# Performance work log

Measured on AMD Instinct MI355X. Metric: run time of the kernel, lower is better.

## Reference

```python
import jax, jax.numpy as jnp
import numpy as np


def _conv(x, w, b=None, pad=0):
    # x: [B,C,H,W], w: [O,I,kh,kw]
    y = jax.lax.conv_general_dilated(
        x, w, window_strides=(1, 1), padding=[(pad, pad), (pad, pad)],
        dimension_numbers=('NCHW', 'OIHW', 'NCHW'))
    if b is not None:
        y = y + b[None, :, None, None]
    return y


def _resb(x, w1, w2):
    h = _conv(x, w1, pad=1)
    h = jax.nn.leaky_relu(h, 0.1)
    h = _conv(h, w2, pad=1)
    return h + x


def setup_inputs() -> dict:
    key = jax.random.key(0)
    ks = jax.random.split(key, 16)
    B, C, H, W, K = 2, 64, 128, 256, 16
    s = 0.05
    return {
        'x_left': jax.random.normal(ks[0], (B, C, H, W), jnp.float32),
        'x_right': jax.random.normal(ks[1], (B, C, H, W), jnp.float32),
        'xxs': jax.random.randint(ks[2], (B, H * W, K), 0, H, jnp.int32),
        'yys': jax.random.randint(ks[3], (B, H * W, K), 0, W, jnp.int32),
        'is_training': 0,
        'rb_w1': jax.random.normal(ks[4], (C, C, 3, 3), jnp.float32) * s,
        'rb_w2': jax.random.normal(ks[5], (C, C, 3, 3), jnp.float32) * s,
        'b1_w': jax.random.normal(ks[6], (C, C, 1, 1), jnp.float32) * s,
        'b1_b': jax.random.normal(ks[7], (C,), jnp.float32) * s,
        'b2_w': jax.random.normal(ks[8], (C, C, 1, 1), jnp.float32) * s,
        'b2_b': jax.random.normal(ks[9], (C,), jnp.float32) * s,
        'b3_w': jax.random.normal(ks[10], (C, C, 1, 1), jnp.float32) * s,
        'b3_b': jax.random.normal(ks[11], (C,), jnp.float32) * s,
        'fus_w': jax.random.normal(ks[12], (C, 2 * C, 1, 1), jnp.float32) * s,
        'fus_b': jax.random.normal(ks[13], (C,), jnp.float32) * s,
    }


def reference(x_left, x_right, xxs, yys, is_training,
              rb_w1, rb_w2, b1_w, b1_b, b2_w, b2_b, b3_w, b3_b, fus_w, fus_b):
    B, C, H, W = x_left.shape
    HW = H * W
    K = xxs.shape[-1]

    buf_l = _resb(x_left, rb_w1, rb_w2)
    buf_r = _resb(x_right, rb_w1, rb_w2)

    Q = _conv(buf_l, b1_w, b1_b)   # [B,C,H,W]
    S = _conv(buf_r, b2_w, b2_b)
    R = _conv(buf_r, b3_w, b3_b)

    # per-pixel gather: S[b,:,Pos_x,Pos_y] -> flat index into H*W
    flat = (xxs.astype(jnp.int32) * W + yys.astype(jnp.int32)).reshape(B, HW * K)  # [B,HW*K]
    Sf = S.reshape(B, C, HW)
    Rf = R.reshape(B, C, HW)
    Key = jnp.take_along_axis(Sf, flat[:, None, :], axis=2).reshape(B, C, HW, K)
    Val = jnp.take_along_axis(Rf, flat[:, None, :], axis=2).reshape(B, C, HW, K)

    Qv = Q.transpose(0, 2, 3, 1).reshape(B, HW, C)           # [B,HW,C]
    score = jnp.einsum('bpc,bcpk->bpk', Qv, Key)             # [B,HW,K]
    M = jax.nn.softmax(score, axis=-1)                       # [B,HW,K]
    buf = jnp.einsum('bpk,bckp->bpc', M, Val.transpose(0, 1, 3, 2))  # [B,HW,C]
    buf = buf.reshape(B, H, W, C).transpose(0, 3, 1, 2)      # [B,C,H,W]

    out = _conv(jnp.concatenate([buf, x_left], axis=1), fus_w, fus_b)
    M_right_to_left = M[:, :, None, :]                       # [B,HW,1,K] as in torch
    if is_training == 1:
        return out
    return (out, M_right_to_left)
```

## Files before the change

### kernel.cpp

```cpp
#include <hip/hip_runtime.h>

#define HH 128
#define WW 256
#define CH 64
#define HWP (HH * WW)

typedef __attribute__((ext_vector_type(8))) __bf16 bf16x8;
typedef __attribute__((ext_vector_type(16))) float float16;

__device__ __forceinline__ unsigned short f2bf(float f) {
    unsigned u = __float_as_uint(f);
    u += 0x7fffu + ((u >> 16) & 1u);
    return (unsigned short)(u >> 16);
}
__device__ __forceinline__ float bf2f(unsigned short u) {
    return __uint_as_float((unsigned)u << 16);
}

__global__ __launch_bounds__(256) void prep_toT_k(
    const float* __restrict__ xl, const float* __restrict__ xr,
    const float* __restrict__ w1, const float* __restrict__ w2,
    const float* __restrict__ b1w, const float* __restrict__ b2w,
    const float* __restrict__ b3w, const float* __restrict__ fusw,
    unsigned short* __restrict__ XT, unsigned short* __restrict__ wB)
{
    const int tid = threadIdx.x;
    if (blockIdx.x < 2048) {
        __shared__ __align__(16) unsigned short sT[64 * 68];
        const int side = blockIdx.x >> 10;
        const int i0   = blockIdx.x & 1023;
        const int gp0  = i0 * 64;
        const int b    = gp0 >> 15;
        const int pofs = gp0 & (HWP - 1);
        const float* in = (side ? xr : xl) + (size_t)b * CH * HWP + pofs;

        for (int i = tid; i < 4096; i += 256) {
            int ci = i >> 6, px = i & 63;
            sT[px * 68 + ci] = f2bf(in[(size_t)ci * HWP + px]);
        }
        __syncthreads();
        const int px = tid >> 2, q = tid & 3;
        unsigned short* op = XT + ((size_t)(side * 2 + b) * HWP + pofs + px) * 64;
#pragma unroll
        for (int r = 0; r < 2; ++r)
            *(uint4*)&op[(q * 2 + r) * 8] = *(uint4*)&sT[px * 68 + (q * 2 + r) * 8];
        return;
    }

    int e = (blockIdx.x - 2048) * 256 + tid;
    float val;
    if (e < 73728) {
        const float* w = (e < 36864) ? w1 : w2;
        int t = (e < 36864) ? e : e - 36864;
        int j = t & 7, L = (t >> 3) & 63, nb = (t >> 9) & 1, kc = t >> 10;
        int k  = kc * 16 + (L >> 5) * 8 + j;
        int n  = nb * 32 + (L & 31);
        int kd = k >> 6, ci = k & 63;
        val = w[(n * 64 + ci) * 9 + kd];
    } else {
        int t = e - 73728;
        if (t < 4096) {
            int j = t & 7, L = (t >> 3) & 63, i3 = t >> 9;
            int nt = i3 & 1, kc = i3 >> 1;
            int n = nt * 32 + (L & 31), k = kc * 16 + (L >> 5) * 8 + j;
            val = b1w[n * 64 + k];
        } else if (t < 12288) {
            t -= 4096;
            int j = t & 7, L = (t >> 3) & 63, i3 = t >> 9;
            int nt = i3 & 3, kc = i3 >> 2;
            int n = nt * 32 + (L & 31), k = kc * 16 + (L >> 5) * 8 + j;
            val = (n < 64) ? b2w[n * 64 + k] : b3w[(n - 64) * 64 + k];
        } else {
            t -= 12288;
            int j = t & 7, L = (t >> 3) & 63, i3 = t >> 9;
            int nt = i3 & 1, kc = i3 >> 1;
            int n = nt * 32 + (L & 31), k = kc * 16 + (L >> 5) * 8 + j;
            val = fusw[n * 128 + k];
        }
    }
    wB[e] = f2bf(val);
}

__device__ __forceinline__ void stage_halo(
    unsigned short* sA, const unsigned short* inT, int x0, int y, int tid)
{
    for (int i = tid; i < 1584; i += 256) {
        int cell = i >> 3, j = i & 7;
        int row = cell / 66, col = cell - row * 66;
        int gy = y + row - 1, gx = x0 + col - 1;
        uint4 v = make_uint4(0, 0, 0, 0);
        if ((unsigned)gy < HH && (unsigned)gx < WW)
            v = *(const uint4*)&inT[(size_t)(gy * WW + gx) * 64 + j * 8];
        *(uint4*)&sA[(row * 66 + col) * 68 + j * 8] = v;
    }
}

__global__ __launch_bounds__(256) void conv1_k(
    const unsigned short* __restrict__ XT, const unsigned short* __restrict__ wB,
    unsigned short* __restrict__ H1T)
{
    __shared__ __align__(16) unsigned short sA[4 * 66 * 68];

    const int tid = threadIdx.x;
    const int x0  = blockIdx.x * 64;
    const int y0  = blockIdx.y * 2;
    const int sb  = blockIdx.z;
    const unsigned short* inT = XT + (size_t)sb * HWP * 64;

    for (int i = tid; i < 2112; i += 256) {
        int cell = i >> 3, j = i & 7;
        int row = cell / 66, col = cell - row * 66;
        int gy = y0 + row - 1, gx = x0 + col - 1;
        uint4 v = make_uint4(0, 0, 0, 0);
        if ((unsigned)gy < HH && (unsigned)gx < WW)
            v = *(const uint4*)&inT[(size_t)(gy * WW + gx) * 64 + j * 8];
        *(uint4*)&sA[(row * 66 + col) * 68 + j * 8] = v;
    }
    __syncthreads();

    const int lane = tid & 63, wv = tid >> 6;
    const int h = wv & 1, nw = wv >> 1;
    const int m = lane & 31, kg = lane >> 5;
    const int pxl = h * 32 + m;

    float16 acc0, acc1;
#pragma unroll
    for (int i = 0; i < 16; ++i) { acc0[i] = 0.f; acc1[i] = 0.f; }

#pragma unroll
    for (int kc = 0; kc < 36; ++kc) {
        const int kd = kc >> 2, hh = kc & 3;
        const int dy = kd / 3, dx = kd - dy * 3;
        bf16x8 bfg = *(const bf16x8*)&wB[((kc * 2 + nw) * 64 + lane) * 8];
        const int base = (dy * 66 + pxl + dx) * 68 + hh * 16 + kg * 8;
        bf16x8 af0 = *(const bf16x8*)&sA[base];
        bf16x8 af1 = *(const bf16x8*)&sA[base + 66 * 68];
        acc0 = __builtin_amdgcn_mfma_f32_32x32x16_bf16(af0, bfg, acc0, 0, 0, 0);
        acc1 = __builtin_amdgcn_mfma_f32_32x32x16_bf16(af1, bfg, acc1, 0, 0, 0);
    }

    __syncthreads();
    unsigned short* sCb = sA;
    const int n = nw * 32 + (lane & 31);
#pragma unroll
    for (int r = 0; r < 16; ++r) {
        int prl = h * 32 + (r & 3) + 8 * (r >> 2) + 4 * kg;
        float v0 = acc0[r]; v0 = v0 > 0.f ? v0 : 0.1f * v0;
        float v1 = acc1[r]; v1 = v1 > 0.f ? v1 : 0.1f * v1;
        sCb[prl * 68 + n] = f2bf(v0);
        sCb[(64 + prl) * 68 + n] = f2bf(v1);
    }
    __syncthreads();

    const int px2 = tid >> 1, q = tid & 1;
    const int rr = px2 >> 6, px = px2 & 63;
    unsigned short* op = H1T + ((size_t)sb * HWP + (y0 + rr) * WW + x0 + px) * 64 + q * 32;
#pragma unroll
    for (int j = 0; j < 4; ++j)
        *(uint4*)&op[j * 8] = *(uint4*)&sCb[px2 * 68 + q * 32 + j * 8];
}

__global__ __launch_bounds__(256) void conv2_k(
    const unsigned short* __restrict__ H1T, const unsigned short* __restrict__ XT,
    const unsigned short* __restrict__ wB2, const unsigned short* __restrict__ wQ,
    const unsigned short* __restrict__ wSR, const float* __restrict__ b1b,
    const float* __restrict__ b2b, const float* __restrict__ b3b,
    unsigned short* __restrict__ QT, unsigned short* __restrict__ ST,
    unsigned short* __restrict__ RT)
{
    __shared__ __align__(16) unsigned short sA[3 * 66 * 68];

    const int tid = threadIdx.x;
    const int x0  = blockIdx.x * 64;
    const int y   = blockIdx.y;
    const int sb  = blockIdx.z;
    const int side = sb >> 1, b = sb & 1;
    const unsigned short* inT = H1T + (size_t)sb * HWP * 64;

    stage_halo(sA, inT, x0, y, tid);
    __syncthreads();

    const int lane = tid & 63, wv = tid >> 6;
    const int mw = wv & 1, nw = wv >> 1;
    const int m = lane & 31, kg = lane >> 5;
    const int px_l = mw * 32 + m;

    float16 acc;
#pragma unroll
    for (int i = 0; i < 16; ++i) acc[i] = 0.f;

#pragma unroll
    for (int kc = 0; kc < 36; ++kc) {
        const int kd = kc >> 2, h = kc & 3;
        const int dy = kd / 3, dx = kd - dy * 3;
        bf16x8 af = *(const bf16x8*)&sA[((dy * 66 + px_l + dx) * 68) + h * 16 + kg * 8];
        bf16x8 bf = *(const bf16x8*)&wB2[((kc * 2 + nw) * 64 + lane) * 8];
        acc = __builtin_amdgcn_mfma_f32_32x32x16_bf16(af, bf, acc, 0, 0, 0);
    }

    __syncthreads();
    unsigned short* sCb = sA;
    unsigned short* sC2 = sA + 4352;
    const int n = nw * 32 + (lane & 31);
    const unsigned short* xres = XT + (size_t)sb * HWP * 64;
#pragma unroll
    for (int r = 0; r < 16; ++r) {
        int pr = mw * 32 + (r & 3) + 8 * (r >> 2) + 4 * kg;
        float xv = bf2f(xres[(size_t)(y * WW + x0 + pr) * 64 + n]);
        sCb[pr * 68 + n] = f2bf(acc[r] + xv);
    }
    __syncthreads();

    if (side == 0) {
        float16 a2;
#pragma unroll
        for (int i = 0; i < 16; ++i) a2[i] = 0.f;
#pragma unroll
        for (int kc = 0; kc < 4; ++kc) {
            bf16x8 af = *(const bf16x8*)&sCb[px_l * 68 + kc * 16 + kg * 8];
            bf16x8 bf = *(const bf16x8*)&wQ[((kc * 2 + nw) * 64 + lane) * 8];
            a2 = __builtin_amdgcn_mfma_f32_32x32x16_bf16(af, bf, a2, 0, 0, 0);
        }
        float bv = b1b[n];
#pragma unroll
        for (int r = 0; r < 16; ++r) {
            int pr = mw * 32 + (r & 3) + 8 * (r >> 2) + 4 * kg;
            sC2[pr * 68 + n] = f2bf(a2[r] + bv);
        }
        __syncthreads();
        const int px = tid >> 2, q = tid & 3;
        unsigned short* op = QT + ((size_t)b * HWP + y * WW + x0 + px) * 64;
#pragma unroll
        for (int r = 0; r < 2; ++r)
            *(uint4*)&op[(q * 2 + r) * 8] = *(uint4*)&sC2[px * 68 + (q * 2 + r) * 8];
    } else {
        float16 a2[2];
#pragma unroll
        for (int t = 0; t < 2; ++t)
#pragma unroll
            for (int i = 0; i < 16; ++i) a2[t][i] = 0.f;
#pragma unroll
        for (int kc = 0; kc < 4; ++kc) {
            bf16x8 af = *(const bf16x8*)&sCb[px_l * 68 + kc * 16 + kg * 8];
#pragma unroll
            for (int t = 0; t < 2; ++t) {
                int nt = nw * 2 + t;
                bf16x8 bf = *(const bf16x8*)&wSR[((kc * 4 + nt) * 64 + lane) * 8];
                a2[t] = __builtin_amdgcn_mfma_f32_32x32x16_bf16(af, bf, a2[t], 0, 0, 0);
            }
        }
#pragma unroll
        for (int t = 0; t < 2; ++t) {
            int nn = (nw * 2 + t) * 32 + (lane & 31);
            float bv = (nn < 64) ? b2b[nn] : b3b[nn - 64];
#pragma unroll
            for (int r = 0; r < 16; ++r) {
                int pr = mw * 32 + (r & 3) + 8 * (r >> 2) + 4 * kg;
                sC2[pr * 132 + nn] = f2bf(a2[t][r] + bv);
            }
        }
        __syncthreads();
        const int px = tid >> 2, q = tid & 3;
        const size_t prow = (size_t)b * HWP + y * WW + x0 + px;
        unsigned short* op = ((q < 2) ? ST : RT) + prow * 64 + (q & 1) * 32;
#pragma unroll
        for (int j = 0; j < 4; ++j)
            *(uint4*)&op[j * 8] = *(uint4*)&sC2[px * 132 + q * 32 + j * 8];
    }
}

__global__ __launch_bounds__(512) void attn_fuse_k(
    const unsigned short* __restrict__ QT, const unsigned short* __restrict__ ST,
    const unsigned short* __restrict__ RT, const int* __restrict__ xxs,
    const int* __restrict__ yys, const unsigned short* __restrict__ XT,
    const unsigned short* __restrict__ wfrag, const float* __restrict__ bias,
    float* __restrict__ out, float* __restrict__ Mout)
{
    __shared__ __align__(16) unsigned char smem[64 * 68 * 4];
    unsigned short* sBuf = (unsigned short*)smem;
    unsigned short* sXT  = (unsigned short*)smem + 64 * 68;
    float*          sC   = (float*)smem;

    const int tid  = threadIdx.x;
    const int lane = tid & 63;
    const int wv   = tid >> 6;

    const int blk = blockIdx.x;
    const int b   = (blk & 4) ? 1 : 0;
    const int sub = (blk >> 3) * 4 + (blk & 3);
    const int pofs = sub * 64;
    const size_t gp0   = (size_t)b * HWP + pofs;
    const size_t bbase = (size_t)b * HWP;

    {
        const unsigned short* xlT = XT + gp0 * 64;
        int px = tid >> 3, j = tid & 7;
        *(uint4*)&sXT[px * 68 + j * 8] = *(const uint4*)&xlT[(size_t)px * 64 + j * 8];
    }

    const int k = lane & 15, cq = lane >> 4;
    for (int it = 0; it < 8; ++it) {
        const int pl = wv * 8 + it;
        const size_t gp = gp0 + pl;

        const int flat = xxs[gp * 16 + k] * WW + yys[gp * 16 + k];

        const unsigned short* srow = ST + (bbase + (size_t)flat) * 64 + cq * 16;
        const unsigned short* qrow = QT + gp * 64 + cq * 16;
        float s = 0.f;
#pragma unroll
        for (int hh = 0; hh < 2; ++hh) {
            uint4 sv = *(const uint4*)(srow + hh * 8);
            uint4 qv = *(const uint4*)(qrow + hh * 8);
            const unsigned* sa = (const unsigned*)&sv;
            const unsigned* qa = (const unsigned*)&qv;
#pragma unroll
            for (int d = 0; d < 4; ++d) {
                s = fmaf(__uint_as_float(sa[d] << 16),
                         __uint_as_float(qa[d] << 16), s);
                s = fmaf(__uint_as_float(sa[d] & 0xffff0000u),
                         __uint_as_float(qa[d] & 0xffff0000u), s);
            }
        }
        s += __shfl_xor(s, 16, 64);
        s += __shfl_xor(s, 32, 64);

        float mx = s;
#pragma unroll
        for (int mm = 1; mm <= 8; mm <<= 1) mx = fmaxf(mx, __shfl_xor(mx, mm, 64));
        const float e = __expf(s - mx);
        float sum = e;
#pragma unroll
        for (int mm = 1; mm <= 8; mm <<= 1) sum += __shfl_xor(sum, mm, 64);
        const float mval = e * (1.f / sum);

        if (lane < 16) Mout[gp * 16 + lane] = mval;

        const unsigned short* rbase = RT + bbase * 64;
        float acc = 0.f;
#pragma unroll
        for (int kk = 0; kk < 16; ++kk) {
            int   fi = __builtin_amdgcn_readlane(flat, kk);
            float mk = __uint_as_float(
                __builtin_amdgcn_readlane(__float_as_uint(mval), kk));
            acc = fmaf(mk, bf2f(rbase[(size_t)fi * 64 + lane]), acc);
        }
        sBuf[pl * 68 + lane] = f2bf(acc);
    }
    __syncthreads();

    float16 facc;
#pragma unroll
    for (int i = 0; i < 16; ++i) facc[i] = 0.f;
    const int mw = wv & 1, nw = (wv >> 1) & 1;
    const int m = lane & 31, kg = lane >> 5;
    const int px_l = mw * 32 + m;

    if (tid < 256) {
#pragma unroll
        for (int kc = 0; kc < 8; ++kc) {
            const unsigned short* asrc = (kc < 4)
                ? &sBuf[px_l * 68 + kc * 16 + kg * 8]
                : &sXT[px_l * 68 + (kc - 4) * 16 + kg * 8];
            bf16x8 af = *(const bf16x8*)asrc;
            bf16x8 bf = *(const bf16x8*)&wfrag[((kc * 2 + nw) * 64 + lane) * 8];
            facc = __builtin_amdgcn_mfma_f32_32x32x16_bf16(af, bf, facc, 0, 0, 0);
        }
    }
    __syncthreads();

    if (tid < 256) {
        const int co_l = nw * 32 + (lane & 31);
#pragma unroll
        for (int r = 0; r < 16; ++r) {
            int pr = mw * 32 + (r & 3) + 8 * (r >> 2) + 4 * kg;
            sC[co_l * 68 + pr] = facc[r];
        }
    }
    __syncthreads();

    if (tid < 256) {
        const int co = tid >> 2, p0 = (tid & 3) * 16;
        const float bv = bias[co];
        float* op = out + ((size_t)b * CH + co) * HWP + pofs + p0;
#pragma unroll
        for (int q = 0; q < 4; ++q) {
            float4 v = *(float4*)&sC[co * 68 + p0 + q * 4];
            v.x += bv; v.y += bv; v.z += bv; v.w += bv;
            *(float4*)&op[q * 4] = v;
        }
    }
}

extern "C" void kernel_launch(void* const* d_in, const int* in_sizes, int n_in,
                              void* d_out, int out_size, void* d_ws, size_t ws_size,
                              hipStream_t stream)
{
    const float* x_left  = (const float*)d_in[0];
    const float* x_right = (const float*)d_in[1];
    const int*   xxs     = (const int*)d_in[2];
    const int*   yys     = (const int*)d_in[3];
    const float* rb_w1   = (const float*)d_in[5];
    const float* rb_w2   = (const float*)d_in[6];
    const float* b1_w    = (const float*)d_in[7];
    const float* b1_b    = (const float*)d_in[8];
    const float* b2_w    = (const float*)d_in[9];
    const float* b2_b    = (const float*)d_in[10];
    const float* b3_w    = (const float*)d_in[11];
    const float* b3_b    = (const float*)d_in[12];
    const float* fus_w   = (const float*)d_in[13];
    const float* fus_b   = (const float*)d_in[14];

    float* out  = (float*)d_out;
    float* Mout = out + (size_t)2 * CH * HWP;

    unsigned short* ws2 = (unsigned short*)d_ws;
    unsigned short* XT   = ws2;
    unsigned short* H1T  = ws2 + 8388608;
    unsigned short* QT   = ws2 + 16777216;
    unsigned short* ST   = ws2 + 20971520;
    unsigned short* RT   = ws2 + 25165824;
    unsigned short* wB   = ws2 + 29360128;

    prep_toT_k<<<2416, 256, 0, stream>>>(x_left, x_right, rb_w1, rb_w2,
                                         b1_w, b2_w, b3_w, fus_w, XT, wB);

    conv1_k<<<dim3(4, 64, 4), 256, 0, stream>>>(XT, wB, H1T);
    conv2_k<<<dim3(4, 128, 4), 256, 0, stream>>>(H1T, XT, wB + 36864, wB + 73728,
                                                 wB + 77824, b1_b, b2_b, b3_b,
                                                 QT, ST, RT);

    attn_fuse_k<<<1024, 512, 0, stream>>>(QT, ST, RT, xxs, yys, XT,
                                          wB + 86016, fus_b, out, Mout);
}
```

Baseline: 197.2 us.

## Use 512-thread blocks with per-wave row split in both 3x3 conv kernels

```diff
diff --git a/kernel.cpp b/kernel.cpp
--- a/kernel.cpp
+++ b/kernel.cpp
@@ -81,33 +81,10 @@
     wB[e] = f2bf(val);
 }
 
-__device__ __forceinline__ void stage_halo(
-    unsigned short* sA, const unsigned short* inT, int x0, int y, int tid)
-{
-    for (int i = tid; i < 1584; i += 256) {
-        int cell = i >> 3, j = i & 7;
-        int row = cell / 66, col = cell - row * 66;
-        int gy = y + row - 1, gx = x0 + col - 1;
-        uint4 v = make_uint4(0, 0, 0, 0);
-        if ((unsigned)gy < HH && (unsigned)gx < WW)
-            v = *(const uint4*)&inT[(size_t)(gy * WW + gx) * 64 + j * 8];
-        *(uint4*)&sA[(row * 66 + col) * 68 + j * 8] = v;
-    }
-}
-
-__global__ __launch_bounds__(256) void conv1_k(
-    const unsigned short* __restrict__ XT, const unsigned short* __restrict__ wB,
-    unsigned short* __restrict__ H1T)
-{
-    __shared__ __align__(16) unsigned short sA[4 * 66 * 68];
-
-    const int tid = threadIdx.x;
-    const int x0  = blockIdx.x * 64;
-    const int y0  = blockIdx.y * 2;
-    const int sb  = blockIdx.z;
-    const unsigned short* inT = XT + (size_t)sb * HWP * 64;
-
-    for (int i = tid; i < 2112; i += 256) {
+__device__ __forceinline__ void stage_halo4(
+    unsigned short* sA, const unsigned short* inT, int x0, int y0, int tid)
+{
+    for (int i = tid; i < 2112; i += 512) {
         int cell = i >> 3, j = i & 7;
         int row = cell / 66, col = cell - row * 66;
         int gy = y0 + row - 1, gx = x0 + col - 1;
@@ -116,27 +93,39 @@
             v = *(const uint4*)&inT[(size_t)(gy * WW + gx) * 64 + j * 8];
         *(uint4*)&sA[(row * 66 + col) * 68 + j * 8] = v;
     }
+}
+
+__global__ __launch_bounds__(512) void conv1_k(
+    const unsigned short* __restrict__ XT, const unsigned short* __restrict__ wB,
+    unsigned short* __restrict__ H1T)
+{
+    __shared__ __align__(16) unsigned short sA[4 * 66 * 68];
+
+    const int tid = threadIdx.x;
+    const int x0  = blockIdx.x * 64;
+    const int y0  = blockIdx.y * 2;
+    const int sb  = blockIdx.z;
+    const unsigned short* inT = XT + (size_t)sb * HWP * 64;
+
+    stage_halo4(sA, inT, x0, y0, tid);
     __syncthreads();
 
     const int lane = tid & 63, wv = tid >> 6;
-    const int h = wv & 1, nw = wv >> 1;
+    const int rr = wv & 1, mw = (wv >> 1) & 1, nw = wv >> 2;
     const int m = lane & 31, kg = lane >> 5;
-    const int pxl = h * 32 + m;
-
-    float16 acc0, acc1;
-#pragma unroll
-    for (int i = 0; i < 16; ++i) { acc0[i] = 0.f; acc1[i] = 0.f; }
+    const int pxl = mw * 32 + m;
+
+    float16 acc;
+#pragma unroll
+    for (int i = 0; i < 16; ++i) acc[i] = 0.f;
 
 #pragma unroll
     for (int kc = 0; kc < 36; ++kc) {
         const int kd = kc >> 2, hh = kc & 3;
         const int dy = kd / 3, dx = kd - dy * 3;
-        bf16x8 bfg = *(const bf16x8*)&wB[((kc * 2 + nw) * 64 + lane) * 8];
-        const int base = (dy * 66 + pxl + dx) * 68 + hh * 16 + kg * 8;
-        bf16x8 af0 = *(const bf16x8*)&sA[base];
-        bf16x8 af1 = *(const bf16x8*)&sA[base + 66 * 68];
-        acc0 = __builtin_amdgcn_mfma_f32_32x32x16_bf16(af0, bfg, acc0, 0, 0, 0);
-        acc1 = __builtin_amdgcn_mfma_f32_32x32x16_bf16(af1, bfg, acc1, 0, 0, 0);
+        bf16x8 af = *(const bf16x8*)&sA[((rr + dy) * 66 + pxl + dx) * 68 + hh * 16 + kg * 8];
+        bf16x8 bf = *(const bf16x8*)&wB[((kc * 2 + nw) * 64 + lane) * 8];
+        acc = __builtin_amdgcn_mfma_f32_32x32x16_bf16(af, bf, acc, 0, 0, 0);
     }
 
     __syncthreads();
@@ -144,23 +133,21 @@
     const int n = nw * 32 + (lane & 31);
 #pragma unroll
     for (int r = 0; r < 16; ++r) {
-        int prl = h * 32 + (r & 3) + 8 * (r >> 2) + 4 * kg;
-        float v0 = acc0[r]; v0 = v0 > 0.f ? v0 : 0.1f * v0;
-        float v1 = acc1[r]; v1 = v1 > 0.f ? v1 : 0.1f * v1;
-        sCb[prl * 68 + n] = f2bf(v0);
-        sCb[(64 + prl) * 68 + n] = f2bf(v1);
-    }
-    __syncthreads();
-
-    const int px2 = tid >> 1, q = tid & 1;
-    const int rr = px2 >> 6, px = px2 & 63;
-    unsigned short* op = H1T + ((size_t)sb * HWP + (y0 + rr) * WW + x0 + px) * 64 + q * 32;
-#pragma unroll
-    for (int j = 0; j < 4; ++j)
-        *(uint4*)&op[j * 8] = *(uint4*)&sCb[px2 * 68 + q * 32 + j * 8];
-}
-
-__global__ __launch_bounds__(256) void conv2_k(
+        int pr = rr * 64 + mw * 32 + (r & 3) + 8 * (r >> 2) + 4 * kg;
+        float v = acc[r];
+        v = v > 0.f ? v : 0.1f * v;
+        sCb[pr * 68 + n] = f2bf(v);
+    }
+    __syncthreads();
+
+    const int px2 = tid >> 2, q = tid & 3;
+    const int orow = px2 >> 6, px = px2 & 63;
+    unsigned short* op = H1T + ((size_t)sb * HWP + (y0 + orow) * WW + x0 + px) * 64 + q * 16;
+    *(uint4*)&op[0] = *(uint4*)&sCb[px2 * 68 + q * 16];
+    *(uint4*)&op[8] = *(uint4*)&sCb[px2 * 68 + q * 16 + 8];
+}
+
+__global__ __launch_bounds__(512) void conv2_k(
     const unsigned short* __restrict__ H1T, const unsigned short* __restrict__ XT,
     const unsigned short* __restrict__ wB2, const unsigned short* __restrict__ wQ,
     const unsigned short* __restrict__ wSR, const float* __restrict__ b1b,
@@ -168,22 +155,22 @@
     unsigned short* __restrict__ QT, unsigned short* __restrict__ ST,
     unsigned short* __restrict__ RT)
 {
-    __shared__ __align__(16) unsigned short sA[3 * 66 * 68];
+    __shared__ __align__(16) unsigned short sA[4 * 66 * 68];
 
     const int tid = threadIdx.x;
     const int x0  = blockIdx.x * 64;
-    const int y   = blockIdx.y;
+    const int y0  = blockIdx.y * 2;
     const int sb  = blockIdx.z;
     const int side = sb >> 1, b = sb & 1;
     const unsigned short* inT = H1T + (size_t)sb * HWP * 64;
 
-    stage_halo(sA, inT, x0, y, tid);
+    stage_halo4(sA, inT, x0, y0, tid);
     __syncthreads();
 
     const int lane = tid & 63, wv = tid >> 6;
-    const int mw = wv & 1, nw = wv >> 1;
+    const int rr = wv & 1, mw = (wv >> 1) & 1, nw = wv >> 2;
     const int m = lane & 31, kg = lane >> 5;
-    const int px_l = mw * 32 + m;
+    const int pxl = mw * 32 + m;
 
     float16 acc;
 #pragma unroll
@@ -191,25 +178,29 @@
 
 #pragma unroll
     for (int kc = 0; kc < 36; ++kc) {
-        const int kd = kc >> 2, h = kc & 3;
+        const int kd = kc >> 2, hh = kc & 3;
         const int dy = kd / 3, dx = kd - dy * 3;
-        bf16x8 af = *(const bf16x8*)&sA[((dy * 66 + px_l + dx) * 68) + h * 16 + kg * 8];
+        bf16x8 af = *(const bf16x8*)&sA[((rr + dy) * 66 + pxl + dx) * 68 + hh * 16 + kg * 8];
         bf16x8 bf = *(const bf16x8*)&wB2[((kc * 2 + nw) * 64 + lane) * 8];
         acc = __builtin_amdgcn_mfma_f32_32x32x16_bf16(af, bf, acc, 0, 0, 0);
     }
 
     __syncthreads();
     unsigned short* sCb = sA;
-    unsigned short* sC2 = sA + 4352;
+    unsigned short* sC2 = sA + 8704;
     const int n = nw * 32 + (lane & 31);
     const unsigned short* xres = XT + (size_t)sb * HWP * 64;
 #pragma unroll
     for (int r = 0; r < 16; ++r) {
-        int pr = mw * 32 + (r & 3) + 8 * (r >> 2) + 4 * kg;
-        float xv = bf2f(xres[(size_t)(y * WW + x0 + pr) * 64 + n]);
+        int pr = rr * 64 + mw * 32 + (r & 3) + 8 * (r >> 2) + 4 * kg;
+        float xv = bf2f(xres[(size_t)((y0 + (pr >> 6)) * WW + x0 + (pr & 63)) * 64 + n]);
         sCb[pr * 68 + n] = f2bf(acc[r] + xv);
     }
     __syncthreads();
+
+    const int px2 = tid >> 2, q = tid & 3;
+    const int orow = px2 >> 6, px = px2 & 63;
+    const size_t prow = (size_t)b * HWP + (y0 + orow) * WW + x0 + px;
 
     if (side == 0) {
         float16 a2;
@@ -217,55 +208,68 @@
         for (int i = 0; i < 16; ++i) a2[i] = 0.f;
 #pragma unroll
         for (int kc = 0; kc < 4; ++kc) {
-            bf16x8 af = *(const bf16x8*)&sCb[px_l * 68 + kc * 16 + kg * 8];
+            bf16x8 af = *(const bf16x8*)&sCb[(rr * 64 + pxl) * 68 + kc * 16 + kg * 8];
             bf16x8 bf = *(const bf16x8*)&wQ[((kc * 2 + nw) * 64 + lane) * 8];
             a2 = __builtin_amdgcn_mfma_f32_32x32x16_bf16(af, bf, a2, 0, 0, 0);
         }
         float bv = b1b[n];
 #pragma unroll
         for (int r = 0; r < 16; ++r) {
-            int pr = mw * 32 + (r & 3) + 8 * (r >> 2) + 4 * kg;
+            int pr = rr * 64 + mw * 32 + (r & 3) + 8 * (r >> 2) + 4 * kg;
             sC2[pr * 68 + n] = f2bf(a2[r] + bv);
         }
         __syncthreads();
-        const int px = tid >> 2, q = tid & 3;
-        unsigned short* op = QT + ((size_t)b * HWP + y * WW + x0 + px) * 64;
-#pragma unroll
-        for (int r = 0; r < 2; ++r)
-            *(uint4*)&op[(q * 2 + r) * 8] = *(uint4*)&sC2[px * 68 + (q * 2 + r) * 8];
+        unsigned short* op = QT + prow * 64 + q * 16;
+        *(uint4*)&op[0] = *(uint4*)&sC2[px2 * 68 + q * 16];
+        *(uint4*)&op[8] = *(uint4*)&sC2[px2 * 68 + q * 16 + 8];
     } else {
-        float16 a2[2];
-#pragma unroll
-        for (int t = 0; t < 2; ++t)
-#pragma unroll
-            for (int i = 0; i < 16; ++i) a2[t][i] = 0.f;
+        float16 a2;
+#pragma unroll
+        for (int i = 0; i < 16; ++i) a2[i] = 0.f;
 #pragma unroll
         for (int kc = 0; kc < 4; ++kc) {
-            bf16x8 af = *(const bf16x8*)&sCb[px_l * 68 + kc * 16 + kg * 8];
-#pragma unroll
-            for (int t = 0; t < 2; ++t) {
-                int nt = nw * 2 + t;
-                bf16x8 bf = *(const bf16x8*)&wSR[((kc * 4 + nt) * 64 + lane) * 8];
-                a2[t] = __builtin_amdgcn_mfma_f32_32x32x16_bf16(af, bf, a2[t], 0, 0, 0);
+            bf16x8 af = *(const bf16x8*)&sCb[(rr * 64 + pxl) * 68 + kc * 16 + kg * 8];
+            bf16x8 bf = *(const bf16x8*)&wSR[((kc * 4 + nw) * 64 + lane) * 8];
+            a2 = __builtin_amdgcn_mfma_f32_32x32x16_bf16(af, bf, a2, 0, 0, 0);
+        }
+        {
+            float bv = b2b[n];
+#pragma unroll
+            for (int r = 0; r < 16; ++r) {
+                int pr = rr * 64 + mw * 32 + (r & 3) + 8 * (r >> 2) + 4 * kg;
+                sC2[pr * 68 + n] = f2bf(a2[r] + bv);
             }
         }
-#pragma unroll
-        for (int t = 0; t < 2; ++t) {
-            int nn = (nw * 2 + t) * 32 + (lane & 31);
-            float bv = (nn < 64) ? b2b[nn] : b3b[nn - 64];
+        __syncthreads();
+        {
+            unsigned short* op = ST + prow * 64 + q * 16;
+            *(uint4*)&op[0] = *(uint4*)&sC2[px2 * 68 + q * 16];
+            *(uint4*)&op[8] = *(uint4*)&sC2[px2 * 68 + q * 16 + 8];
+        }
+        __syncthreads();
+
+#pragma unroll
+        for (int i = 0; i < 16; ++i) a2[i] = 0.f;
+#pragma unroll
+        for (int kc = 0; kc < 4; ++kc) {
+            bf16x8 af = *(const bf16x8*)&sCb[(rr * 64 + pxl) * 68 + kc * 16 + kg * 8];
+            bf16x8 bf = *(const bf16x8*)&wSR[((kc * 4 + 2 + nw) * 64 + lane) * 8];
+            a2 = __builtin_amdgcn_mfma_f32_32x32x16_bf16(af, bf, a2, 0, 0, 0);
+        }
+        {
+            float bv = b3b[n];
 #pragma unroll
             for (int r = 0; r < 16; ++r) {
-                int pr = mw * 32 + (r & 3) + 8 * (r >> 2) + 4 * kg;
-                sC2[pr * 132 + nn] = f2bf(a2[t][r] + bv);
+                int pr = rr * 64 + mw * 32 + (r & 3) + 8 * (r >> 2) + 4 * kg;
+                sC2[pr * 68 + n] = f2bf(a2[r] + bv);
             }
         }
         __syncthreads();
-        const int px = tid >> 2, q = tid & 3;
-        const size_t prow = (size_t)b * HWP + y * WW + x0 + px;
-        unsigned short* op = ((q < 2) ? ST : RT) + prow * 64 + (q & 1) * 32;
-#pragma unroll
-        for (int j = 0; j < 4; ++j)
-            *(uint4*)&op[j * 8] = *(uint4*)&sC2[px * 132 + q * 32 + j * 8];
+        {
+            unsigned short* op = RT + prow * 64 + q * 16;
+            *(uint4*)&op[0] = *(uint4*)&sC2[px2 * 68 + q * 16];
+            *(uint4*)&op[8] = *(uint4*)&sC2[px2 * 68 + q * 16 + 8];
+        }
     }
 }
 
@@ -425,10 +429,10 @@
     prep_toT_k<<<2416, 256, 0, stream>>>(x_left, x_right, rb_w1, rb_w2,
                                          b1_w, b2_w, b3_w, fus_w, XT, wB);
 
-    conv1_k<<<dim3(4, 64, 4), 256, 0, stream>>>(XT, wB, H1T);
-    conv2_k<<<dim3(4, 128, 4), 256, 0, stream>>>(H1T, XT, wB + 36864, wB + 73728,
-                                                 wB + 77824, b1_b, b2_b, b3_b,
-                                                 QT, ST, RT);
+    conv1_k<<<dim3(4, 64, 4), 512, 0, stream>>>(XT, wB, H1T);
+    conv2_k<<<dim3(4, 64, 4), 512, 0, stream>>>(H1T, XT, wB + 36864, wB + 73728,
+                                                wB + 77824, b1_b, b2_b, b3_b,
+                                                QT, ST, RT);
 
     attn_fuse_k<<<1024, 512, 0, stream>>>(QT, ST, RT, xxs, yys, XT,
                                           wB + 86016, fus_b, out, Mout);
```

After: 192.1 us. 2.6% less time.
